# Optimization experiments

Measured on AMD Instinct MI355X. Metric: run time of the kernel, lower is better.

Reference implementation:

```python
import math
import jax, jax.numpy as jnp
import numpy as np

H = 8      # head_count
M = 9      # box window over key positions (odd)
N = 3      # box window over key heads (odd)


def _box(x, w, axis):
    """Sliding box-sum of width w with SAME padding ((w-1)//2 each side).
    Mathematically identical to F.conv1d with an all-ones kernel of size w."""
    p = (w - 1) // 2
    pad = [(0, 0)] * x.ndim
    pad[axis] = (p, p)
    xp = jnp.pad(x, pad)
    c = jnp.cumsum(xp, axis=axis)
    pad2 = [(0, 0)] * x.ndim
    pad2[axis] = (1, 0)
    c = jnp.pad(c, pad2)
    n = x.shape[axis]
    hi = jax.lax.slice_in_dim(c, w, w + n, axis=axis)
    lo = jax.lax.slice_in_dim(c, 0, n, axis=axis)
    return hi - lo


def _scatter_idx(b, h, q, k, m, n):
    """Flat destination indices reproducing torch masked_scatter_ semantics:
    source elements are consumed in flat order and written to masked slots."""
    hw = (n - 1) // 2
    pw = (m - 1) // 2
    hi = np.arange(h)
    head_mask = np.abs(hi[:, None] - hi[None, :]) <= hw          # (h, h)
    qi = np.arange(q)
    ki = np.arange(k)
    pos_mask = np.abs(qi[:, None] - ki[None, :]) <= pw           # (q, k)
    mw = head_mask[:, None, :, None] | pos_mask[None, :, None, :]  # (h,q,h,k)
    flat = np.flatnonzero(mw.reshape(-1)).astype(np.int64)
    per = h * q * h * k
    idx = (np.arange(b, dtype=np.int64)[:, None] * per + flat[None, :]).reshape(-1)
    return idx


def setup_inputs() -> dict:
    key = jax.random.key(0)
    ks = jax.random.split(key, 12)
    B, S, D = 2, 512, 512
    sc = 1.0 / math.sqrt(D)
    inp = {
        "key_in": jax.random.normal(ks[0], (B, S, D), jnp.float32),
        "value_in": jax.random.normal(ks[1], (B, S, D), jnp.float32),
        "query_in": jax.random.normal(ks[2], (B, S, D), jnp.float32),
        "mask": jax.random.bernoulli(ks[3], 0.05, (B, S, S)),
        "Wq": jax.random.normal(ks[4], (D, D), jnp.float32) * sc,
        "bq": jnp.zeros((D,), jnp.float32),
        "Wk": jax.random.normal(ks[5], (D, D), jnp.float32) * sc,
        "bk": jnp.zeros((D,), jnp.float32),
        "Wv": jax.random.normal(ks[6], (D, D), jnp.float32) * sc,
        "bv": jnp.zeros((D,), jnp.float32),
        "Wo": jax.random.normal(ks[7], (D, D), jnp.float32) * sc,
        "bo": jnp.zeros((D,), jnp.float32),
    }
    return inp


def reference(key_in, value_in, query_in, mask, Wq, bq, Wk, bk, Wv, bv, Wo, bo):
    B, S, D = key_in.shape
    h = H
    dh = D // h

    def proj(x, W, b):
        # nn.Linear then shape(): (B, S, D) -> (B, h, S, dh)
        return (x @ W.T + b).reshape(B, S, h, dh).transpose(0, 2, 1, 3)

    q = proj(query_in, Wq, bq) / math.sqrt(dh)
    k = proj(key_in, Wk, bk)
    v = proj(value_in, Wv, bv)

    qf = q.reshape(B, h * S, dh)
    kf = k.reshape(B, h * S, dh)
    vf = v.reshape(B, h * S, dh)

    # cross-head scores: (B, H*Sq, H*Sk) viewed as (B, qh, q, kh, k)
    scores = jnp.einsum("bid,bjd->bij", qf, kf).astype(jnp.float32)
    scores = scores.reshape(B, h, S, h, S)
    scores = jnp.where(mask[:, None, :, None, :], jnp.float32(-1e18), scores)

    # convolSoftmax: exp then box-normalize over a (N kh) x (M kpos) window
    e = jnp.exp(scores)                       # (B, qh, q, kh, k)
    denom = _box(_box(e, M, axis=4), N, axis=3)
    attn = (e / denom).astype(query_in.dtype)

    # masked_scatter_: attn elements in flat order -> masked slots of zeros
    idx = jnp.asarray(_scatter_idx(B, h, S, S, M, N))
    flat = attn.reshape(-1)
    attn_masked = jnp.zeros_like(flat).at[idx].set(flat[: idx.shape[0]])
    attn_masked = attn_masked.reshape(B, h * S, h * S)

    ctx = jnp.einsum("bij,bjd->bid", attn_masked, vf)   # (B, H*S, dh)
    # faithful 'unshape' on the 3D tensor: transpose(1,2) then view(B,-1,H*dh)
    ctx = jnp.transpose(ctx, (0, 2, 1)).reshape(B, S, h * dh)
    out = ctx @ Wo.T + bo

    top_attn = attn[:, 0, :, 0, :]
    return out, top_attn
```

## Files before the change

### kernel.cpp

```cpp
#include <hip/hip_runtime.h>
#include <math.h>


__global__ void zero_kernel(int* __restrict__ flags)
{
    if (threadIdx.x < 2) flags[threadIdx.x] = 0;
}

__global__ __launch_bounds__(256) void detect_kernel(const unsigned int* __restrict__ mask_words,
                                                     int* __restrict__ flags)
{
    __shared__ int sh[2];
    if (threadIdx.x == 0) { sh[0] = 0; sh[1] = 0; }
    __syncthreads();
    int bad_int = 0, bad_f32 = 0;
    int base = blockIdx.x * 2048;
    for (int t = threadIdx.x; t < 2048; t += 256) {
        unsigned w = mask_words[base + t];
        if (w > 1u) bad_int = 1;
        if (w != 0u && w != 0x3F800000u) bad_f32 = 1;
    }
    if (bad_int) atomicOr(&sh[0], 1);
    if (bad_f32) atomicOr(&sh[1], 1);
    __syncthreads();
    if (threadIdx.x == 0) {
        if (sh[0]) atomicOr(&flags[0], 1);
        if (sh[1]) atomicOr(&flags[1], 1);
    }
}

__global__ __launch_bounds__(256) void proj3_kernel(const float* __restrict__ Xq, const float* __restrict__ Xk,
                                                    const float* __restrict__ Xv,
                                                    const float* __restrict__ Wq, const float* __restrict__ Wk,
                                                    const float* __restrict__ Wv,
                                                    const float* __restrict__ bq, const float* __restrict__ bk,
                                                    const float* __restrict__ bv,
                                                    float* __restrict__ dq, float* __restrict__ dk,
                                                    float* __restrict__ dv)
{
    const float* X; const float* W; const float* bias; float* dst; float scale;
    if (blockIdx.z == 0)      { X = Xq; W = Wq; bias = bq; dst = dq; scale = 0.125f; }
    else if (blockIdx.z == 1) { X = Xk; W = Wk; bias = bk; dst = dk; scale = 1.0f; }
    else                      { X = Xv; W = Wv; bias = bv; dst = dv; scale = 1.0f; }

    __shared__ float As[2][32][68], Bs[2][32][68];
    int tid = threadIdx.x;
    int tx = tid & 15, ty = tid >> 4;
    int r0 = blockIdx.y * 64, o0 = blockIdx.x * 64;
    int sr = tid >> 2, sc = (tid & 3) * 8;
    const float* Xp = X + (size_t)(r0 + sr) * 512 + sc;
    const float* Wp = W + (size_t)(o0 + sr) * 512 + sc;

    float4 pa0, pa1, pb0, pb1;
#define P3_LOAD(K0) { \
        pa0 = *reinterpret_cast<const float4*>(Xp + (K0)); \
        pa1 = *reinterpret_cast<const float4*>(Xp + (K0) + 4); \
        pb0 = *reinterpret_cast<const float4*>(Wp + (K0)); \
        pb1 = *reinterpret_cast<const float4*>(Wp + (K0) + 4); }
#define P3_WRITE(BUF) { \
        As[BUF][sc + 0][sr] = pa0.x; As[BUF][sc + 1][sr] = pa0.y; \
        As[BUF][sc + 2][sr] = pa0.z; As[BUF][sc + 3][sr] = pa0.w; \
        As[BUF][sc + 4][sr] = pa1.x; As[BUF][sc + 5][sr] = pa1.y; \
        As[BUF][sc + 6][sr] = pa1.z; As[BUF][sc + 7][sr] = pa1.w; \
        Bs[BUF][sc + 0][sr] = pb0.x; Bs[BUF][sc + 1][sr] = pb0.y; \
        Bs[BUF][sc + 2][sr] = pb0.z; Bs[BUF][sc + 3][sr] = pb0.w; \
        Bs[BUF][sc + 4][sr] = pb1.x; Bs[BUF][sc + 5][sr] = pb1.y; \
        Bs[BUF][sc + 6][sr] = pb1.z; Bs[BUF][sc + 7][sr] = pb1.w; }

    P3_LOAD(0);
    P3_WRITE(0);
    P3_LOAD(32);

    float acc[4][4] = {};
    int cur = 0;
    for (int s = 0; s < 16; ++s) {
        __syncthreads();
#pragma unroll
        for (int kk = 0; kk < 32; ++kk) {
            float4 a = *reinterpret_cast<const float4*>(&As[cur][kk][ty * 4]);
            float4 bv = *reinterpret_cast<const float4*>(&Bs[cur][kk][tx * 4]);
            acc[0][0] = fmaf(a.x, bv.x, acc[0][0]); acc[0][1] = fmaf(a.x, bv.y, acc[0][1]);
            acc[0][2] = fmaf(a.x, bv.z, acc[0][2]); acc[0][3] = fmaf(a.x, bv.w, acc[0][3]);
            acc[1][0] = fmaf(a.y, bv.x, acc[1][0]); acc[1][1] = fmaf(a.y, bv.y, acc[1][1]);
            acc[1][2] = fmaf(a.y, bv.z, acc[1][2]); acc[1][3] = fmaf(a.y, bv.w, acc[1][3]);
            acc[2][0] = fmaf(a.z, bv.x, acc[2][0]); acc[2][1] = fmaf(a.z, bv.y, acc[2][1]);
            acc[2][2] = fmaf(a.z, bv.z, acc[2][2]); acc[2][3] = fmaf(a.z, bv.w, acc[2][3]);
            acc[3][0] = fmaf(a.w, bv.x, acc[3][0]); acc[3][1] = fmaf(a.w, bv.y, acc[3][1]);
            acc[3][2] = fmaf(a.w, bv.z, acc[3][2]); acc[3][3] = fmaf(a.w, bv.w, acc[3][3]);
        }
        if (s + 1 < 16) {
            P3_WRITE(cur ^ 1);
            if (s + 2 < 16) P3_LOAD((s + 2) * 32);
        }
        cur ^= 1;
    }

#pragma unroll
    for (int i = 0; i < 4; ++i) {
        int r = r0 + ty * 4 + i;
        int b = r >> 9, s = r & 511;
#pragma unroll
        for (int j = 0; j < 4; ++j) {
            int o = o0 + tx * 4 + j;
            float v = (acc[i][j] + bias[o]) * scale;
            dst[(((size_t)b * 8 + (o >> 6)) * 512 + s) * 64 + (o & 63)] = v;
        }
    }
}

__global__ __launch_bounds__(256) void scores_kernel(const float* __restrict__ qh, const float* __restrict__ kh,
                                                     float* __restrict__ scores)
{
    __shared__ float As[64][68], Bs[64][68];
    int tid = threadIdx.x;
    int r0 = blockIdx.y * 64, c0 = blockIdx.x * 64;
    int b1 = (r0 >= 3072);
    const float* Ab = qh + (b1 ? (size_t)1024 * 64 : 0);
    const float* Bb = kh + (b1 ? (size_t)4096 * 64 : 0);
    int sr = tid >> 2, sc = (tid & 3) * 16;
    {
        const float* Ap = Ab + (size_t)(r0 + sr) * 64 + sc;
        const float* Bp = Bb + (size_t)(c0 + sr) * 64 + sc;
#pragma unroll
        for (int l = 0; l < 4; ++l) {
            float4 a = *reinterpret_cast<const float4*>(Ap + l * 4);
            float4 b = *reinterpret_cast<const float4*>(Bp + l * 4);
            As[sc + l * 4 + 0][sr] = a.x; As[sc + l * 4 + 1][sr] = a.y;
            As[sc + l * 4 + 2][sr] = a.z; As[sc + l * 4 + 3][sr] = a.w;
            Bs[sc + l * 4 + 0][sr] = b.x; Bs[sc + l * 4 + 1][sr] = b.y;
            Bs[sc + l * 4 + 2][sr] = b.z; Bs[sc + l * 4 + 3][sr] = b.w;
        }
    }
    __syncthreads();
    int tx = tid & 15, ty = tid >> 4;
    float acc[4][4] = {};
#pragma unroll 8
    for (int kk = 0; kk < 64; ++kk) {
        float4 a = *reinterpret_cast<const float4*>(&As[kk][ty * 4]);
        float4 bv = *reinterpret_cast<const float4*>(&Bs[kk][tx * 4]);
        acc[0][0] = fmaf(a.x, bv.x, acc[0][0]); acc[0][1] = fmaf(a.x, bv.y, acc[0][1]);
        acc[0][2] = fmaf(a.x, bv.z, acc[0][2]); acc[0][3] = fmaf(a.x, bv.w, acc[0][3]);
        acc[1][0] = fmaf(a.y, bv.x, acc[1][0]); acc[1][1] = fmaf(a.y, bv.y, acc[1][1]);
        acc[1][2] = fmaf(a.y, bv.z, acc[1][2]); acc[1][3] = fmaf(a.y, bv.w, acc[1][3]);
        acc[2][0] = fmaf(a.z, bv.x, acc[2][0]); acc[2][1] = fmaf(a.z, bv.y, acc[2][1]);
        acc[2][2] = fmaf(a.z, bv.z, acc[2][2]); acc[2][3] = fmaf(a.z, bv.w, acc[2][3]);
        acc[3][0] = fmaf(a.w, bv.x, acc[3][0]); acc[3][1] = fmaf(a.w, bv.y, acc[3][1]);
        acc[3][2] = fmaf(a.w, bv.z, acc[3][2]); acc[3][3] = fmaf(a.w, bv.w, acc[3][3]);
    }
#pragma unroll
    for (int i = 0; i < 4; ++i)
#pragma unroll
        for (int j = 0; j < 4; ++j)
            scores[(size_t)(r0 + ty * 4 + i) * 4096 + (c0 + tx * 4 + j)] = acc[i][j];
}

#define EIDX(h, k) (((h) * 544) + (k) + ((k) >> 4))
__global__ __launch_bounds__(256) void attn_kernel(float* __restrict__ scores, const void* __restrict__ mask,
                                                   const int* __restrict__ flags, float* __restrict__ top_out)
{
    __shared__ float e[8 * 544];
    int row = blockIdx.x;
    int b = (row >= 3072);
    int hq = b ? 0 : (row >> 9);
    int q  = b ? (row - 3072) : (row & 511);
    float* rp = scores + (size_t)row * 4096;
    int mode = (!flags[0]) ? 0 : ((!flags[1]) ? 2 : 1);
    int t = threadIdx.x;
    int hk = t >> 5;
    int k0 = (t & 31) << 4;
    int j0 = (hk << 9) + k0;
    size_t mrow = ((size_t)b * 512 + q) * 512 + k0;

    float sv[16];
    {
        const float4* p4 = reinterpret_cast<const float4*>(rp + j0);
#pragma unroll
        for (int l = 0; l < 4; ++l) {
            float4 v = p4[l];
            sv[l * 4 + 0] = v.x; sv[l * 4 + 1] = v.y; sv[l * 4 + 2] = v.z; sv[l * 4 + 3] = v.w;
        }
    }
    bool mv[16];
    if (mode == 0) {
        const int4* mp = reinterpret_cast<const int4*>((const int*)mask + mrow);
#pragma unroll
        for (int l = 0; l < 4; ++l) {
            int4 w = mp[l];
            mv[l * 4 + 0] = w.x != 0; mv[l * 4 + 1] = w.y != 0;
            mv[l * 4 + 2] = w.z != 0; mv[l * 4 + 3] = w.w != 0;
        }
    } else if (mode == 2) {
        const float4* mp = reinterpret_cast<const float4*>((const float*)mask + mrow);
#pragma unroll
        for (int l = 0; l < 4; ++l) {
            float4 w = mp[l];
            mv[l * 4 + 0] = w.x != 0.0f; mv[l * 4 + 1] = w.y != 0.0f;
            mv[l * 4 + 2] = w.z != 0.0f; mv[l * 4 + 3] = w.w != 0.0f;
        }
    } else {
        uint4 w = *reinterpret_cast<const uint4*>((const unsigned char*)mask + mrow);
        unsigned int ws[4] = {w.x, w.y, w.z, w.w};
#pragma unroll
        for (int i = 0; i < 16; ++i) mv[i] = ((ws[i >> 2] >> ((i & 3) * 8)) & 0xFFu) != 0u;
    }

    float ev[16];
#pragma unroll
    for (int i = 0; i < 16; ++i) ev[i] = mv[i] ? 0.0f : __expf(sv[i]);
#pragma unroll
    for (int i = 0; i < 16; ++i) e[EIDX(hk, k0 + i)] = ev[i];
    __syncthreads();

    float d[16] = {};
#pragma unroll
    for (int dr = -1; dr <= 1; ++dr) {
        int hh = hk + dr;
        if (hh < 0 || hh > 7) continue;
        float w24[24];
#pragma unroll
        for (int p = 0; p < 24; ++p) {
            int kk = k0 + p - 4;
            w24[p] = (kk >= 0 && kk < 512) ? e[EIDX(hh, kk)] : 0.0f;
        }
        float pr[25];
        pr[0] = 0.0f;
#pragma unroll
        for (int p = 0; p < 24; ++p) pr[p + 1] = pr[p] + w24[p];
#pragma unroll
        for (int i = 0; i < 16; ++i) d[i] += pr[i + 9] - pr[i];
    }

    float av[16];
#pragma unroll
    for (int i = 0; i < 16; ++i) av[i] = ev[i] / d[i];

    {
        float4* p4 = reinterpret_cast<float4*>(rp + j0);
#pragma unroll
        for (int l = 0; l < 4; ++l) {
            float4 v;
            v.x = av[l * 4 + 0]; v.y = av[l * 4 + 1]; v.z = av[l * 4 + 2]; v.w = av[l * 4 + 3];
            p4[l] = v;
        }
    }
    if (hq == 0 && hk == 0) {
        float4* p4 = reinterpret_cast<float4*>(top_out + mrow);
#pragma unroll
        for (int l = 0; l < 4; ++l) {
            float4 v;
            v.x = av[l * 4 + 0]; v.y = av[l * 4 + 1]; v.z = av[l * 4 + 2]; v.w = av[l * 4 + 3];
            p4[l] = v;
        }
    }
}

__global__ __launch_bounds__(256) void ctx_kernel(const float* __restrict__ attn_src, const float* __restrict__ vh,
                                                  float* __restrict__ ctxT, float* __restrict__ part1,
                                                  float* __restrict__ part2)
{
    __shared__ float As[2][32][34];
    __shared__ float Vs[2][32][64];
    __shared__ int rowOff[32];

    int tid = threadIdx.x;
    int tx = tid & 15;
    int ty = tid >> 4;
    int q0 = blockIdx.x * 32;
    int hq = blockIdx.y;
    int bz = blockIdx.z;
    int b = bz / 3;
    int ks = bz % 3;

    int hkLo = (hq - 1 < 0) ? 0 : hq - 1;
    int hkHi = (hq + 1 > 7) ? 7 : hq + 1;
    int nband = hkHi - hkLo + 1;
    float* dst = (ks == 0) ? ctxT : ((ks == 1) ? part1 : part2);

    if (ks >= nband) {
#pragma unroll
        for (int i = 0; i < 2; ++i) {
            int q = q0 + ty * 2 + i;
#pragma unroll
            for (int j = 0; j < 4; ++j)
                dst[((size_t)b * 512 + (tx * 4 + j) * 8 + hq) * 512 + q] = 0.0f;
        }
        return;
    }

    if (tid < 32) {
        int q = q0 + tid;
        int A = (hq > 0) ? (551816 + (hq - 1) * 809372) : 0;
        int nHP = (hq == 0 || hq == 7) ? 2 : 3;
        int s1 = (q >= 5) ? 10 : (4 * q - (q * (q - 1)) / 2);
        int s2 = (q <= 508) ? 0 : ((q - 508) * (q - 507)) / 2;
        int pref = 9 * q - s1 - s2;
        int rb = A + nHP * 512 * q + (8 - nHP) * pref;
        int lo = (q - 4 < 0) ? 0 : q - 4;
        int hi = (q + 4 > 511) ? 511 : q + 4;
        rowOff[tid] = b * 5959864 + rb + hkLo * (hi - lo + 1);
    }
    __syncthreads();

    int ac = tid & 31;
    int aq = tid >> 5;
    int ro[4];
#pragma unroll
    for (int l = 0; l < 4; ++l) ro[l] = rowOff[aq + 8 * l];
    int vr = tid >> 4, vc = (tid & 15) * 4;
    int hk = hkLo + ks;
    int bandAdd = ks << 9;
    const float* vb = vh + (((size_t)b * 8 + hk) * 512) * 64;

    float pa[4]; float4 pv[2];
#define CTX_LOAD(S) { \
        int kk0_ = (S) << 5; \
        _Pragma("unroll") \
        for (int l = 0; l < 4; ++l) pa[l] = attn_src[ro[l] + bandAdd + kk0_ + ac]; \
        _Pragma("unroll") \
        for (int l = 0; l < 2; ++l) \
            pv[l] = *reinterpret_cast<const float4*>(vb + (size_t)(kk0_ + vr + 16 * l) * 64 + vc); \
    }
#define CTX_WRITE(BUF) { \
        _Pragma("unroll") \
        for (int l = 0; l < 4; ++l) As[BUF][ac][aq + 8 * l] = pa[l]; \
        _Pragma("unroll") \
        for (int l = 0; l < 2; ++l) \
            *reinterpret_cast<float4*>(&Vs[BUF][vr + 16 * l][vc]) = pv[l]; \
    }

    CTX_LOAD(0);
    CTX_WRITE(0);
    CTX_LOAD(1);

    float acc[2][4] = {};
    int ty2 = ty * 2;
    int cur = 0;
    for (int s = 0; s < 16; ++s) {
        __syncthreads();
#pragma unroll
        for (int kk = 0; kk < 32; ++kk) {
            float2 a = *reinterpret_cast<const float2*>(&As[cur][kk][ty2]);
            float4 v = *reinterpret_cast<const float4*>(&Vs[cur][kk][tx * 4]);
            acc[0][0] = fmaf(a.x, v.x, acc[0][0]); acc[0][1] = fmaf(a.x, v.y, acc[0][1]);
            acc[0][2] = fmaf(a.x, v.z, acc[0][2]); acc[0][3] = fmaf(a.x, v.w, acc[0][3]);
            acc[1][0] = fmaf(a.y, v.x, acc[1][0]); acc[1][1] = fmaf(a.y, v.y, acc[1][1]);
            acc[1][2] = fmaf(a.y, v.z, acc[1][2]); acc[1][3] = fmaf(a.y, v.w, acc[1][3]);
        }
        if (s + 1 < 16) {
            CTX_WRITE(cur ^ 1);
            if (s + 2 < 16) CTX_LOAD(s + 2);
        }
        cur ^= 1;
    }

    if (ks == 0) {
#pragma unroll
        for (int i = 0; i < 2; ++i) {
            int q = q0 + ty2 + i;
            int lo = (q - 4 < 0) ? 0 : q - 4;
            int hi = (q + 4 > 511) ? 511 : q + 4;
            int cnt = hi - lo + 1;
            int cOff = rowOff[ty2 + i] - hkLo * cnt;
            int t = 0;
            for (int hh = 0; hh < 8; ++hh) {
                if (hh >= hkLo && hh <= hkHi) { t += 512; continue; }
                const float* vbase = vh + (((size_t)b * 8 + hh) * 512) * 64 + tx * 4;
                for (int k = lo; k <= hi; ++k) {
                    float a = attn_src[cOff + t]; ++t;
                    const float4 v = *reinterpret_cast<const float4*>(vbase + (size_t)k * 64);
                    acc[i][0] = fmaf(a, v.x, acc[i][0]);
                    acc[i][1] = fmaf(a, v.y, acc[i][1]);
                    acc[i][2] = fmaf(a, v.z, acc[i][2]);
                    acc[i][3] = fmaf(a, v.w, acc[i][3]);
                }
            }
        }
    }

#pragma unroll
    for (int i = 0; i < 2; ++i) {
        int q = q0 + ty2 + i;
#pragma unroll
        for (int j = 0; j < 4; ++j)
            dst[((size_t)b * 512 + (tx * 4 + j) * 8 + hq) * 512 + q] = acc[i][j];
    }
}

__global__ __launch_bounds__(256) void out_kernel(const float* __restrict__ ctxT, const float* __restrict__ part1,
                                                  const float* __restrict__ part2,
                                                  const float* __restrict__ Wo,
                                                  const float* __restrict__ bo, float* __restrict__ out)
{
    __shared__ float As[2][32][68], Bs[2][32][68];
    int tid = threadIdx.x;
    int b = blockIdx.z;
    int r0 = blockIdx.y * 64, o0 = blockIdx.x * 64;
    int tx = tid & 15, ty = tid >> 4;
    int sr = tid >> 2, sc = (tid & 3) * 8;
    const float* Ap = ctxT + (size_t)b * 262144 + (size_t)(r0 + sr) * 512 + sc;
    const float* P1p = part1 + (size_t)b * 262144 + (size_t)(r0 + sr) * 512 + sc;
    const float* P2p = part2 + (size_t)b * 262144 + (size_t)(r0 + sr) * 512 + sc;
    const float* Wp = Wo + (size_t)(o0 + sr) * 512 + sc;

    float4 pa0, pa1, pb0, pb1;
#define OUT_LOAD(K0) { \
        float4 a0 = *reinterpret_cast<const float4*>(Ap + (K0)); \
        float4 a1 = *reinterpret_cast<const float4*>(Ap + (K0) + 4); \
        float4 q0v = *reinterpret_cast<const float4*>(P1p + (K0)); \
        float4 q1v = *reinterpret_cast<const float4*>(P1p + (K0) + 4); \
        float4 r0v = *reinterpret_cast<const float4*>(P2p + (K0)); \
        float4 r1v = *reinterpret_cast<const float4*>(P2p + (K0) + 4); \
        pa0.x = a0.x + q0v.x + r0v.x; pa0.y = a0.y + q0v.y + r0v.y; \
        pa0.z = a0.z + q0v.z + r0v.z; pa0.w = a0.w + q0v.w + r0v.w; \
        pa1.x = a1.x + q1v.x + r1v.x; pa1.y = a1.y + q1v.y + r1v.y; \
        pa1.z = a1.z + q1v.z + r1v.z; pa1.w = a1.w + q1v.w + r1v.w; \
        pb0 = *reinterpret_cast<const float4*>(Wp + (K0)); \
        pb1 = *reinterpret_cast<const float4*>(Wp + (K0) + 4); }

    OUT_LOAD(0);
    P3_WRITE(0);
    OUT_LOAD(32);

    float acc[4][4] = {};
    int cur = 0;
    for (int s = 0; s < 16; ++s) {
        __syncthreads();
#pragma unroll
        for (int kk = 0; kk < 32; ++kk) {
            float4 a = *reinterpret_cast<const float4*>(&As[cur][kk][ty * 4]);
            float4 bv = *reinterpret_cast<const float4*>(&Bs[cur][kk][tx * 4]);
            acc[0][0] = fmaf(a.x, bv.x, acc[0][0]); acc[0][1] = fmaf(a.x, bv.y, acc[0][1]);
            acc[0][2] = fmaf(a.x, bv.z, acc[0][2]); acc[0][3] = fmaf(a.x, bv.w, acc[0][3]);
            acc[1][0] = fmaf(a.y, bv.x, acc[1][0]); acc[1][1] = fmaf(a.y, bv.y, acc[1][1]);
            acc[1][2] = fmaf(a.y, bv.z, acc[1][2]); acc[1][3] = fmaf(a.y, bv.w, acc[1][3]);
            acc[2][0] = fmaf(a.z, bv.x, acc[2][0]); acc[2][1] = fmaf(a.z, bv.y, acc[2][1]);
            acc[2][2] = fmaf(a.z, bv.z, acc[2][2]); acc[2][3] = fmaf(a.z, bv.w, acc[2][3]);
            acc[3][0] = fmaf(a.w, bv.x, acc[3][0]); acc[3][1] = fmaf(a.w, bv.y, acc[3][1]);
            acc[3][2] = fmaf(a.w, bv.z, acc[3][2]); acc[3][3] = fmaf(a.w, bv.w, acc[3][3]);
        }
        if (s + 1 < 16) {
            P3_WRITE(cur ^ 1);
            if (s + 2 < 16) OUT_LOAD((s + 2) * 32);
        }
        cur ^= 1;
    }

#pragma unroll
    for (int i = 0; i < 4; ++i) {
        int r = r0 + ty * 4 + i;
#pragma unroll
        for (int j = 0; j < 4; ++j) {
            int o = o0 + tx * 4 + j;
            out[((size_t)b * 512 + r) * 512 + o] = acc[i][j] + bo[o];
        }
    }
}

extern "C" void kernel_launch(void* const* d_in, const int* in_sizes, int n_in,
                              void* d_out, int out_size, void* d_ws, size_t ws_size,
                              hipStream_t stream)
{
    const float* key_in   = (const float*)d_in[0];
    const float* value_in = (const float*)d_in[1];
    const float* query_in = (const float*)d_in[2];
    const void*  mask     = d_in[3];
    const float* Wq = (const float*)d_in[4];
    const float* bq = (const float*)d_in[5];
    const float* Wk = (const float*)d_in[6];
    const float* bk = (const float*)d_in[7];
    const float* Wv = (const float*)d_in[8];
    const float* bv = (const float*)d_in[9];
    const float* Wo = (const float*)d_in[10];
    const float* bo = (const float*)d_in[11];

    float* ws = (float*)d_ws;
    float* qh = ws;
    float* kh = qh + 524288;
    float* vh = kh + 524288;
    float* scores = vh + 524288;
    float* ctxT = scores + 14680064;
    int* flags = (int*)(ctxT + 524288);

    float* out = (float*)d_out;
    float* top = out + 524288;

    zero_kernel<<<1, 64, 0, stream>>>(flags);
    detect_kernel<<<64, 256, 0, stream>>>((const unsigned int*)mask, flags);
    proj3_kernel<<<dim3(8, 16, 3), 256, 0, stream>>>(query_in, key_in, value_in,
                                                     Wq, Wk, Wv, bq, bk, bv, qh, kh, vh);
    scores_kernel<<<dim3(64, 56), 256, 0, stream>>>(qh, kh, scores);
    attn_kernel<<<3584, 256, 0, stream>>>(scores, mask, flags, top);
    ctx_kernel<<<dim3(16, 8, 6), 256, 0, stream>>>(scores, vh, ctxT, qh, kh);
    out_kernel<<<dim3(8, 8, 2), 256, 0, stream>>>(ctxT, qh, kh, Wo, bo, out);
}
```

Before: 268.3 us.

## Retile ctx kernel to 64-query blocks with 4x8 register tiles and vector IO

The ctx kernel now handles 64 queries per block with 128 threads, and each thread computes a 4x8 output tile instead of 2x4. Attention rows are loaded as float4 vectors and transposed into shared memory, and outputs are written as float4 along the query dimension instead of scalar strided stores. This raises arithmetic intensity per shared-memory load and coalesces the global traffic. In exchange the grid halves to 384 blocks of 128 threads, which may leave the GPU underfilled, and the As transpose writes may hit LDS bank conflicts.

```diff
diff --git a/kernel.cpp b/kernel.cpp
--- a/kernel.cpp
+++ b/kernel.cpp
@@ -254,18 +254,18 @@
     }
 }
 
-__global__ __launch_bounds__(256) void ctx_kernel(const float* __restrict__ attn_src, const float* __restrict__ vh,
+__global__ __launch_bounds__(128) void ctx_kernel(const float* __restrict__ attn_src, const float* __restrict__ vh,
                                                   float* __restrict__ ctxT, float* __restrict__ part1,
                                                   float* __restrict__ part2)
 {
-    __shared__ float As[2][32][34];
-    __shared__ float Vs[2][32][64];
-    __shared__ int rowOff[32];
+    __shared__ float As[2][32][68];
+    __shared__ float Vs[2][32][68];
+    __shared__ int rowOff[64];
 
     int tid = threadIdx.x;
     int tx = tid & 15;
     int ty = tid >> 4;
-    int q0 = blockIdx.x * 32;
+    int q0 = blockIdx.x * 64;
     int hq = blockIdx.y;
     int bz = blockIdx.z;
     int b = bz / 3;
@@ -277,17 +277,16 @@
     float* dst = (ks == 0) ? ctxT : ((ks == 1) ? part1 : part2);
 
     if (ks >= nband) {
-#pragma unroll
-        for (int i = 0; i < 2; ++i) {
-            int q = q0 + ty * 2 + i;
-#pragma unroll
-            for (int j = 0; j < 4; ++j)
-                dst[((size_t)b * 512 + (tx * 4 + j) * 8 + hq) * 512 + q] = 0.0f;
+        float4 z = {0.f, 0.f, 0.f, 0.f};
+#pragma unroll
+        for (int j = 0; j < 8; ++j) {
+            int d = ty * 8 + j;
+            *reinterpret_cast<float4*>(&dst[((size_t)b * 512 + d * 8 + hq) * 512 + q0 + tx * 4]) = z;
         }
         return;
     }
 
-    if (tid < 32) {
+    if (tid < 64) {
         int q = q0 + tid;
         int A = (hq > 0) ? (551816 + (hq - 1) * 809372) : 0;
         int nHP = (hq == 0 || hq == 7) ? 2 : 3;
@@ -301,50 +300,56 @@
     }
     __syncthreads();
 
-    int ac = tid & 31;
-    int aq = tid >> 5;
-    int ro[4];
-#pragma unroll
-    for (int l = 0; l < 4; ++l) ro[l] = rowOff[aq + 8 * l];
-    int vr = tid >> 4, vc = (tid & 15) * 4;
+    int wq = tid & 63;
+    int wk0 = (tid >> 6) * 16;
+    int aro = rowOff[wq];
+    int vd = tid & 15, vk = tid >> 4;
+    int bandAdd = ks << 9;
     int hk = hkLo + ks;
-    int bandAdd = ks << 9;
     const float* vb = vh + (((size_t)b * 8 + hk) * 512) * 64;
 
-    float pa[4]; float4 pv[2];
+    float pa[16]; float4 pv[4];
 #define CTX_LOAD(S) { \
         int kk0_ = (S) << 5; \
+        const float* ap_ = attn_src + aro + bandAdd + kk0_ + wk0; \
+        float4 a0_ = *reinterpret_cast<const float4*>(ap_); \
+        float4 a1_ = *reinterpret_cast<const float4*>(ap_ + 4); \
+        float4 a2_ = *reinterpret_cast<const float4*>(ap_ + 8); \
+        float4 a3_ = *reinterpret_cast<const float4*>(ap_ + 12); \
+        pa[0] = a0_.x; pa[1] = a0_.y; pa[2] = a0_.z; pa[3] = a0_.w; \
+        pa[4] = a1_.x; pa[5] = a1_.y; pa[6] = a1_.z; pa[7] = a1_.w; \
+        pa[8] = a2_.x; pa[9] = a2_.y; pa[10] = a2_.z; pa[11] = a2_.w; \
+        pa[12] = a3_.x; pa[13] = a3_.y; pa[14] = a3_.z; pa[15] = a3_.w; \
         _Pragma("unroll") \
-        for (int l = 0; l < 4; ++l) pa[l] = attn_src[ro[l] + bandAdd + kk0_ + ac]; \
-        _Pragma("unroll") \
-        for (int l = 0; l < 2; ++l) \
-            pv[l] = *reinterpret_cast<const float4*>(vb + (size_t)(kk0_ + vr + 16 * l) * 64 + vc); \
-    }
+        for (int l = 0; l < 4; ++l) \
+            pv[l] = *reinterpret_cast<const float4*>(vb + (size_t)(kk0_ + vk + 8 * l) * 64 + vd * 4); }
 #define CTX_WRITE(BUF) { \
         _Pragma("unroll") \
-        for (int l = 0; l < 4; ++l) As[BUF][ac][aq + 8 * l] = pa[l]; \
+        for (int i = 0; i < 16; ++i) As[BUF][wk0 + i][wq] = pa[i]; \
         _Pragma("unroll") \
-        for (int l = 0; l < 2; ++l) \
-            *reinterpret_cast<float4*>(&Vs[BUF][vr + 16 * l][vc]) = pv[l]; \
-    }
+        for (int l = 0; l < 4; ++l) \
+            *reinterpret_cast<float4*>(&Vs[BUF][vk + 8 * l][vd * 4]) = pv[l]; }
 
     CTX_LOAD(0);
     CTX_WRITE(0);
     CTX_LOAD(1);
 
-    float acc[2][4] = {};
-    int ty2 = ty * 2;
+    float acc[4][8] = {};
     int cur = 0;
     for (int s = 0; s < 16; ++s) {
         __syncthreads();
 #pragma unroll
         for (int kk = 0; kk < 32; ++kk) {
-            float2 a = *reinterpret_cast<const float2*>(&As[cur][kk][ty2]);
-            float4 v = *reinterpret_cast<const float4*>(&Vs[cur][kk][tx * 4]);
-            acc[0][0] = fmaf(a.x, v.x, acc[0][0]); acc[0][1] = fmaf(a.x, v.y, acc[0][1]);
-            acc[0][2] = fmaf(a.x, v.z, acc[0][2]); acc[0][3] = fmaf(a.x, v.w, acc[0][3]);
-            acc[1][0] = fmaf(a.y, v.x, acc[1][0]); acc[1][1] = fmaf(a.y, v.y, acc[1][1]);
-            acc[1][2] = fmaf(a.y, v.z, acc[1][2]); acc[1][3] = fmaf(a.y, v.w, acc[1][3]);
+            float4 a = *reinterpret_cast<const float4*>(&As[cur][kk][tx * 4]);
+            float4 v0 = *reinterpret_cast<const float4*>(&Vs[cur][kk][ty * 8]);
+            float4 v1 = *reinterpret_cast<const float4*>(&Vs[cur][kk][ty * 8 + 4]);
+            float av_[4] = {a.x, a.y, a.z, a.w};
+            float vv_[8] = {v0.x, v0.y, v0.z, v0.w, v1.x, v1.y, v1.z, v1.w};
+#pragma unroll
+            for (int i = 0; i < 4; ++i)
+#pragma unroll
+                for (int j = 0; j < 8; ++j)
+                    acc[i][j] = fmaf(av_[i], vv_[j], acc[i][j]);
         }
         if (s + 1 < 16) {
             CTX_WRITE(cur ^ 1);
@@ -355,34 +360,35 @@
 
     if (ks == 0) {
 #pragma unroll
-        for (int i = 0; i < 2; ++i) {
-            int q = q0 + ty2 + i;
+        for (int i = 0; i < 4; ++i) {
+            int q = q0 + tx * 4 + i;
             int lo = (q - 4 < 0) ? 0 : q - 4;
             int hi = (q + 4 > 511) ? 511 : q + 4;
             int cnt = hi - lo + 1;
-            int cOff = rowOff[ty2 + i] - hkLo * cnt;
+            int cOff = rowOff[tx * 4 + i] - hkLo * cnt;
             int t = 0;
             for (int hh = 0; hh < 8; ++hh) {
                 if (hh >= hkLo && hh <= hkHi) { t += 512; continue; }
-                const float* vbase = vh + (((size_t)b * 8 + hh) * 512) * 64 + tx * 4;
+                const float* vbase = vh + (((size_t)b * 8 + hh) * 512) * 64 + ty * 8;
                 for (int k = lo; k <= hi; ++k) {
                     float a = attn_src[cOff + t]; ++t;
-                    const float4 v = *reinterpret_cast<const float4*>(vbase + (size_t)k * 64);
-                    acc[i][0] = fmaf(a, v.x, acc[i][0]);
-                    acc[i][1] = fmaf(a, v.y, acc[i][1]);
-                    acc[i][2] = fmaf(a, v.z, acc[i][2]);
-                    acc[i][3] = fmaf(a, v.w, acc[i][3]);
+                    const float4 v0 = *reinterpret_cast<const float4*>(vbase + (size_t)k * 64);
+                    const float4 v1 = *reinterpret_cast<const float4*>(vbase + (size_t)k * 64 + 4);
+                    acc[i][0] = fmaf(a, v0.x, acc[i][0]); acc[i][1] = fmaf(a, v0.y, acc[i][1]);
+                    acc[i][2] = fmaf(a, v0.z, acc[i][2]); acc[i][3] = fmaf(a, v0.w, acc[i][3]);
+                    acc[i][4] = fmaf(a, v1.x, acc[i][4]); acc[i][5] = fmaf(a, v1.y, acc[i][5]);
+                    acc[i][6] = fmaf(a, v1.z, acc[i][6]); acc[i][7] = fmaf(a, v1.w, acc[i][7]);
                 }
             }
         }
     }
 
 #pragma unroll
-    for (int i = 0; i < 2; ++i) {
-        int q = q0 + ty2 + i;
-#pragma unroll
-        for (int j = 0; j < 4; ++j)
-            dst[((size_t)b * 512 + (tx * 4 + j) * 8 + hq) * 512 + q] = acc[i][j];
+    for (int j = 0; j < 8; ++j) {
+        int d = ty * 8 + j;
+        float4 o;
+        o.x = acc[0][j]; o.y = acc[1][j]; o.z = acc[2][j]; o.w = acc[3][j];
+        *reinterpret_cast<float4*>(&dst[((size_t)b * 512 + d * 8 + hq) * 512 + q0 + tx * 4]) = o;
     }
 }
 
@@ -490,6 +496,6 @@
                                                      Wq, Wk, Wv, bq, bk, bv, qh, kh, vh);
     scores_kernel<<<dim3(64, 56), 256, 0, stream>>>(qh, kh, scores);
     attn_kernel<<<3584, 256, 0, stream>>>(scores, mask, flags, top);
-    ctx_kernel<<<dim3(16, 8, 6), 256, 0, stream>>>(scores, vh, ctxT, qh, kh);
+    ctx_kernel<<<dim3(8, 8, 6), 128, 0, stream>>>(scores, vh, ctxT, qh, kh);
     out_kernel<<<dim3(8, 8, 2), 256, 0, stream>>>(ctxT, qh, kh, Wo, bo, out);
 }
```

Result: slower. 325.3 us (+21.3%).
